# Optimization experiments

Hardware: AMD Instinct MI355X
Metric: run time of the kernel (lower is better)

## Reference

```python
import jax, jax.numpy as jnp
import numpy as np

B, S, ENC_H, DEC_H, ATTN = 64, 2048, 512, 512, 512


def setup_inputs() -> dict:
    key = jax.random.key(0)
    k1, k2, k3, k4, k5 = jax.random.split(key, 5)
    enc_outputs = jax.random.normal(k1, (B, S, ENC_H), dtype=jnp.float32)
    dec_hidden = jax.random.normal(k2, (B, DEC_H), dtype=jnp.float32)
    # nn.Linear(in, out, bias=False): weight shape [out, in]; y = x @ W.T
    s_enc = 1.0 / np.sqrt(ENC_H)
    s_dec = 1.0 / np.sqrt(DEC_H)
    s_v = 1.0 / np.sqrt(ATTN)
    W_enc = jax.random.uniform(k3, (ATTN, ENC_H), minval=-s_enc, maxval=s_enc, dtype=jnp.float32)
    W_dec = jax.random.uniform(k4, (ATTN, DEC_H), minval=-s_dec, maxval=s_dec, dtype=jnp.float32)
    v = jax.random.uniform(k5, (1, ATTN), minval=-s_v, maxval=s_v, dtype=jnp.float32)
    return {"enc_outputs": enc_outputs, "dec_hidden": dec_hidden,
            "W_enc": W_enc, "W_dec": W_dec, "v": v}


def reference(enc_outputs, dec_hidden, W_enc, W_dec, v):
    # enc_proj: [B,S,A], dec_proj: [B,1,A]
    enc_proj = jnp.einsum('bse,ae->bsa', enc_outputs, W_enc)
    dec_proj = jnp.einsum('bd,ad->ba', dec_hidden, W_dec)[:, None, :]
    score = jnp.einsum('bsa,a->bs', jnp.tanh(enc_proj + dec_proj), v[0])  # [B,S]
    attn_weights = jax.nn.softmax(score, axis=1)
    context = jnp.einsum('bs,bse->be', attn_weights, enc_outputs)  # [B,ENC_H]
    return (context, attn_weights)
```

## Files before the change

### kernel.cpp

```cpp
#include <hip/hip_runtime.h>
#include <hip/hip_bf16.h>

#define B_N 64
#define S_N 2048
#define E_N 512
#define A_N 512

typedef __bf16 bf16x8 __attribute__((ext_vector_type(8)));
typedef float  f32x4  __attribute__((ext_vector_type(4)));

__device__ __forceinline__ unsigned short f2bf(float f) {
  return __builtin_bit_cast(unsigned short, (__bf16)f);
}

__global__ void k_convw(const float* __restrict__ W, unsigned short* __restrict__ Wbf) {
  const int i = (blockIdx.x * 256 + threadIdx.x) * 4;
  const float4 v = *(const float4*)(W + i);
  ushort4 p;
  p.x = f2bf(v.x); p.y = f2bf(v.y); p.z = f2bf(v.z); p.w = f2bf(v.w);
  *(ushort4*)(Wbf + i) = p;
}

__global__ __launch_bounds__(256) void k_decproj(const float* __restrict__ dh,
                                                 const float* __restrict__ Wd,
                                                 float* __restrict__ decp) {
  const int b = blockIdx.x, tid = threadIdx.x;
  __shared__ float h[E_N];
  h[tid] = dh[b * E_N + tid];
  h[tid + 256] = dh[b * E_N + 256 + tid];
  __syncthreads();
  for (int a = tid; a < A_N; a += 256) {
    const float* wr = Wd + (size_t)a * E_N;
    float s = 0.f;
    #pragma unroll 8
    for (int e = 0; e < E_N; e += 4) {
      const float4 w4 = *(const float4*)(wr + e);
      s += w4.x * h[e] + w4.y * h[e + 1] + w4.z * h[e + 2] + w4.w * h[e + 3];
    }
    decp[b * A_N + a] = s;
  }
}

#define A_SZb   (64 * 128)
#define B_SZb   (512 * 128)
#define RED_OFF (A_SZb + B_SZb)
#define LDS_TOT (A_SZb + B_SZb + 4 * 64 * 4)

__device__ __forceinline__ int a_off(int r, int cb) {
  return r * 128 + (cb ^ ((r & 7) << 4));
}
__device__ __forceinline__ int b_off(int r, int cb) {
  return A_SZb + r * 128 + (cb ^ ((r & 7) << 4));
}

__global__ __launch_bounds__(256, 2) void k_scores(
    const float* __restrict__ enc, const unsigned short* __restrict__ Wbf,
    const float* __restrict__ decp, const float* __restrict__ vvec,
    float* __restrict__ scores) {
  __shared__ __align__(16) unsigned char lds[LDS_TOT];
  const int tid = threadIdx.x;
  const int lane = tid & 63, wv = tid >> 6, q = lane >> 4, ln = lane & 15;
  const int m0 = blockIdx.x * 64;
  const int b  = m0 >> 11;

  f32x4 acc[4][8] = {};

  for (int ks = 0; ks < 8; ++ks) {
    const int k0 = ks * 64;
    __syncthreads();
    {
      const float* Ag = enc + (size_t)m0 * E_N + k0;
      #pragma unroll
      for (int i = 0; i < 4; ++i) {
        const int idx = i * 256 + tid;
        const int row = idx >> 4, c = idx & 15;
        const float4 v4 = *(const float4*)(Ag + (size_t)row * E_N + c * 4);
        ushort4 p;
        p.x = f2bf(v4.x); p.y = f2bf(v4.y); p.z = f2bf(v4.z); p.w = f2bf(v4.w);
        *(ushort4*)(lds + a_off(row, c * 8)) = p;
      }
    }
    {
      const unsigned short* Wg = Wbf + k0;
      #pragma unroll
      for (int i = 0; i < 16; ++i) {
        const int idx = i * 256 + tid;
        const int row = idx >> 3, c = idx & 7;
        const uint4 v4 = *(const uint4*)(Wg + (size_t)row * A_N + c * 8);
        *(uint4*)(lds + b_off(row, c * 16)) = v4;
      }
    }
    __syncthreads();
    #pragma unroll
    for (int kt = 0; kt < 2; ++kt) {
      bf16x8 af[4], bfr[8];
      #pragma unroll
      for (int mt = 0; mt < 4; ++mt)
        af[mt] = *(const bf16x8*)(lds + a_off(mt * 16 + ln, kt * 64 + q * 16));
      #pragma unroll
      for (int nt = 0; nt < 8; ++nt)
        bfr[nt] = *(const bf16x8*)(lds + b_off(wv * 128 + nt * 16 + ln, kt * 64 + q * 16));
      #pragma unroll
      for (int mt = 0; mt < 4; ++mt) {
        #pragma unroll
        for (int nt = 0; nt < 8; ++nt)
          acc[mt][nt] = __builtin_amdgcn_mfma_f32_16x16x32_bf16(af[mt], bfr[nt], acc[mt][nt], 0, 0, 0);
      }
    }
  }

  float vv[8], dp[8];
  #pragma unroll
  for (int nt = 0; nt < 8; ++nt) {
    const int a = wv * 128 + nt * 16 + ln;
    vv[nt] = vvec[a];
    dp[nt] = decp[b * A_N + a];
  }
  float part[4][4] = {};
  #pragma unroll
  for (int mt = 0; mt < 4; ++mt) {
    #pragma unroll
    for (int nt = 0; nt < 8; ++nt) {
      #pragma unroll
      for (int r = 0; r < 4; ++r) {
        float x = acc[mt][nt][r] + dp[nt];
        x = fminf(9.f, fmaxf(-9.f, x));
        const float ex = __expf(2.f * x);
        part[mt][r] = fmaf(__fdividef(ex - 1.f, ex + 1.f), vv[nt], part[mt][r]);
      }
    }
  }
  float* red = (float*)(lds + RED_OFF);
  #pragma unroll
  for (int mt = 0; mt < 4; ++mt) {
    #pragma unroll
    for (int r = 0; r < 4; ++r) {
      float s = part[mt][r];
      s += __shfl_xor(s, 1);
      s += __shfl_xor(s, 2);
      s += __shfl_xor(s, 4);
      s += __shfl_xor(s, 8);
      if (ln == 0) red[wv * 64 + mt * 16 + q * 4 + r] = s;
    }
  }
  __syncthreads();
  if (tid < 64)
    scores[m0 + tid] = red[tid] + red[64 + tid] + red[128 + tid] + red[192 + tid];
}

__global__ __launch_bounds__(256) void k_softmax(const float* __restrict__ scores,
                                                 float* __restrict__ attn) {
  const int b = blockIdx.x, tid = threadIdx.x;
  float l[8];
  float mx = -3.4e38f;
  #pragma unroll
  for (int i = 0; i < 8; ++i) {
    l[i] = scores[b * S_N + i * 256 + tid];
    mx = fmaxf(mx, l[i]);
  }
  #pragma unroll
  for (int m = 1; m < 64; m <<= 1) mx = fmaxf(mx, __shfl_xor(mx, m));
  __shared__ float sred[8];
  if ((tid & 63) == 0) sred[tid >> 6] = mx;
  __syncthreads();
  mx = fmaxf(fmaxf(sred[0], sred[1]), fmaxf(sred[2], sred[3]));
  float se = 0.f;
  #pragma unroll
  for (int i = 0; i < 8; ++i) { l[i] = __expf(l[i] - mx); se += l[i]; }
  #pragma unroll
  for (int m = 1; m < 64; m <<= 1) se += __shfl_xor(se, m);
  if ((tid & 63) == 0) sred[4 + (tid >> 6)] = se;
  __syncthreads();
  se = sred[4] + sred[5] + sred[6] + sred[7];
  const float inv = 1.f / se;
  #pragma unroll
  for (int i = 0; i < 8; ++i) attn[b * S_N + i * 256 + tid] = l[i] * inv;
}

__global__ __launch_bounds__(512) void k_context(const float* __restrict__ enc,
                                                 const float* __restrict__ attn,
                                                 float* __restrict__ ctx) {
  const int blk = blockIdx.x;
  const int b = blk >> 2, eq = blk & 3;
  const int tid = threadIdx.x;
  const int te = tid & 31, sg = tid >> 5;
  const int e0 = eq * 128 + te * 4;
  const float* ep = enc + (size_t)b * S_N * E_N + e0;
  const float* wp = attn + b * S_N;
  f32x4 acc = {0.f, 0.f, 0.f, 0.f};
  const int s0 = sg * 128;
  #pragma unroll 4
  for (int s = s0; s < s0 + 128; ++s) {
    const float w = wp[s];
    const f32x4 ev = *(const f32x4*)(ep + (size_t)s * E_N);
    acc += w * ev;
  }
  __shared__ f32x4 red[16][32];
  red[sg][te] = acc;
  __syncthreads();
  if (sg == 0) {
    f32x4 t = red[0][te];
    #pragma unroll
    for (int g = 1; g < 16; ++g) t += red[g][te];
    *(f32x4*)(ctx + (size_t)b * E_N + e0) = t;
  }
}

extern "C" void kernel_launch(void* const* d_in, const int* in_sizes, int n_in,
                              void* d_out, int out_size, void* d_ws, size_t ws_size,
                              hipStream_t stream) {
  const float* enc = (const float*)d_in[0];
  const float* dh  = (const float*)d_in[1];
  const float* We  = (const float*)d_in[2];
  const float* Wd  = (const float*)d_in[3];
  const float* v   = (const float*)d_in[4];

  float* out_ctx  = (float*)d_out;
  float* out_attn = out_ctx + B_N * E_N;

  float* scores = (float*)d_ws;
  float* decp   = scores + B_N * S_N;
  unsigned short* Wbf = (unsigned short*)(decp + B_N * A_N);

  k_convw  <<<256, 256, 0, stream>>>(We, Wbf);
  k_decproj<<<B_N, 256, 0, stream>>>(dh, Wd, decp);
  k_scores <<<(B_N * S_N) / 64, 256, 0, stream>>>(enc, Wbf, decp, v, scores);
  k_softmax<<<B_N, 256, 0, stream>>>(scores, out_attn);
  k_context<<<B_N * 4, 512, 0, stream>>>(enc, out_attn, out_ctx);
}
```

Before: 211.7 us.

## Pre-pack W_enc into MFMA fragment layout and double-buffer the A tile

W_enc is now converted to bf16 directly in the per-lane MFMA operand order, so k_scores loads its B fragments straight from global memory (L2-resident) and no longer stages the 64KB weight tile through LDS each k-step. The encoder tile is double-buffered in LDS, with the next slice prefetched into registers while MFMAs run, which removes one barrier per iteration. Blocks grow to 512 threads (8 waves, each covering 64 attention columns), which shrinks the per-wave accumulators and LDS use. The cost is repeated global/L2 loads of the weight fragments by every block, plus more waves contending for them.

Result: slower. 227.2 us (+7.3%).

```diff
diff --git a/kernel.cpp b/kernel.cpp
--- a/kernel.cpp
+++ b/kernel.cpp
@@ -9,16 +9,25 @@
 typedef __bf16 bf16x8 __attribute__((ext_vector_type(8)));
 typedef float  f32x4  __attribute__((ext_vector_type(4)));
 
-__device__ __forceinline__ unsigned short f2bf(float f) {
-  return __builtin_bit_cast(unsigned short, (__bf16)f);
-}
-
-__global__ void k_convw(const float* __restrict__ W, unsigned short* __restrict__ Wbf) {
-  const int i = (blockIdx.x * 256 + threadIdx.x) * 4;
-  const float4 v = *(const float4*)(W + i);
-  ushort4 p;
-  p.x = f2bf(v.x); p.y = f2bf(v.y); p.z = f2bf(v.z); p.w = f2bf(v.w);
-  *(ushort4*)(Wbf + i) = p;
+__device__ __forceinline__ unsigned int f2bfu(float f) {
+  return (unsigned int)__builtin_bit_cast(unsigned short, (__bf16)f);
+}
+
+__global__ __launch_bounds__(256) void k_pack(const float* __restrict__ W,
+                                              unsigned short* __restrict__ Wp) {
+  const int pk = blockIdx.x * 256 + threadIdx.x;
+  const int l = pk & 63, k32 = (pk >> 6) & 15, c = pk >> 10;
+  const int ln = l & 15, q = l >> 4;
+  const int a = c * 16 + ln, k = k32 * 32 + q * 8;
+  const float* src = W + (size_t)a * E_N + k;
+  const float4 u = *(const float4*)src;
+  const float4 w = *(const float4*)(src + 4);
+  uint4 o;
+  o.x = f2bfu(u.x) | (f2bfu(u.y) << 16);
+  o.y = f2bfu(u.z) | (f2bfu(u.w) << 16);
+  o.z = f2bfu(w.x) | (f2bfu(w.y) << 16);
+  o.w = f2bfu(w.z) | (f2bfu(w.w) << 16);
+  *(uint4*)(Wp + (size_t)pk * 8) = o;
 }
 
 __global__ __launch_bounds__(256) void k_decproj(const float* __restrict__ dh,
@@ -41,20 +50,15 @@
   }
 }
 
-#define A_SZb   (64 * 128)
-#define B_SZb   (512 * 128)
-#define RED_OFF (A_SZb + B_SZb)
-#define LDS_TOT (A_SZb + B_SZb + 4 * 64 * 4)
-
-__device__ __forceinline__ int a_off(int r, int cb) {
-  return r * 128 + (cb ^ ((r & 7) << 4));
-}
-__device__ __forceinline__ int b_off(int r, int cb) {
-  return A_SZb + r * 128 + (cb ^ ((r & 7) << 4));
-}
-
-__global__ __launch_bounds__(256, 2) void k_scores(
-    const float* __restrict__ enc, const unsigned short* __restrict__ Wbf,
+#define RED_OFF (2 * 8192)
+#define LDS_TOT (2 * 8192 + 8 * 64 * 4)
+
+__device__ __forceinline__ int a_off(int p, int r, int cb) {
+  return p * 8192 + r * 128 + (cb ^ ((r & 7) << 4));
+}
+
+__global__ __launch_bounds__(512, 2) void k_scores(
+    const float* __restrict__ enc, const unsigned short* __restrict__ Wp,
     const float* __restrict__ decp, const float* __restrict__ vvec,
     float* __restrict__ scores) {
   __shared__ __align__(16) unsigned char lds[LDS_TOT];
@@ -62,65 +66,76 @@
   const int lane = tid & 63, wv = tid >> 6, q = lane >> 4, ln = lane & 15;
   const int m0 = blockIdx.x * 64;
   const int b  = m0 >> 11;
-
-  f32x4 acc[4][8] = {};
+  const bf16x8* __restrict__ Wp16 = (const bf16x8*)Wp;
+
+  const int srow = tid >> 3, sc8 = (tid & 7) * 8, scb = (tid & 7) * 16;
+  const float* Arow = enc + (size_t)m0 * E_N + (size_t)srow * E_N + sc8;
+
+  {
+    const float4 u = *(const float4*)Arow;
+    const float4 w = *(const float4*)(Arow + 4);
+    uint4 o;
+    o.x = f2bfu(u.x) | (f2bfu(u.y) << 16);
+    o.y = f2bfu(u.z) | (f2bfu(u.w) << 16);
+    o.z = f2bfu(w.x) | (f2bfu(w.y) << 16);
+    o.w = f2bfu(w.z) | (f2bfu(w.w) << 16);
+    *(uint4*)(lds + a_off(0, srow, scb)) = o;
+  }
+
+  f32x4 acc[4][4] = {};
 
   for (int ks = 0; ks < 8; ++ks) {
-    const int k0 = ks * 64;
     __syncthreads();
-    {
-      const float* Ag = enc + (size_t)m0 * E_N + k0;
-      #pragma unroll
-      for (int i = 0; i < 4; ++i) {
-        const int idx = i * 256 + tid;
-        const int row = idx >> 4, c = idx & 15;
-        const float4 v4 = *(const float4*)(Ag + (size_t)row * E_N + c * 4);
-        ushort4 p;
-        p.x = f2bf(v4.x); p.y = f2bf(v4.y); p.z = f2bf(v4.z); p.w = f2bf(v4.w);
-        *(ushort4*)(lds + a_off(row, c * 8)) = p;
+    const int p = ks & 1;
+    float4 u, w;
+    if (ks < 7) {
+      u = *(const float4*)(Arow + (ks + 1) * 64);
+      w = *(const float4*)(Arow + (ks + 1) * 64 + 4);
+    }
+    bf16x8 bfr[2][4];
+    #pragma unroll
+    for (int kt = 0; kt < 2; ++kt) {
+      #pragma unroll
+      for (int nt = 0; nt < 4; ++nt) {
+        const int c = wv * 4 + nt;
+        bfr[kt][nt] = Wp16[(c * 16 + ks * 2 + kt) * 64 + lane];
       }
     }
-    {
-      const unsigned short* Wg = Wbf + k0;
-      #pragma unroll
-      for (int i = 0; i < 16; ++i) {
-        const int idx = i * 256 + tid;
-        const int row = idx >> 3, c = idx & 7;
-        const uint4 v4 = *(const uint4*)(Wg + (size_t)row * A_N + c * 8);
-        *(uint4*)(lds + b_off(row, c * 16)) = v4;
-      }
-    }
-    __syncthreads();
-    #pragma unroll
-    for (int kt = 0; kt < 2; ++kt) {
-      bf16x8 af[4], bfr[8];
+    bf16x8 afr[2][4];
+    #pragma unroll
+    for (int kt = 0; kt < 2; ++kt)
       #pragma unroll
       for (int mt = 0; mt < 4; ++mt)
-        af[mt] = *(const bf16x8*)(lds + a_off(mt * 16 + ln, kt * 64 + q * 16));
-      #pragma unroll
-      for (int nt = 0; nt < 8; ++nt)
-        bfr[nt] = *(const bf16x8*)(lds + b_off(wv * 128 + nt * 16 + ln, kt * 64 + q * 16));
-      #pragma unroll
-      for (int mt = 0; mt < 4; ++mt) {
+        afr[kt][mt] = *(const bf16x8*)(lds + a_off(p, mt * 16 + ln, kt * 64 + q * 16));
+    #pragma unroll
+    for (int kt = 0; kt < 2; ++kt)
+      #pragma unroll
+      for (int mt = 0; mt < 4; ++mt)
         #pragma unroll
-        for (int nt = 0; nt < 8; ++nt)
-          acc[mt][nt] = __builtin_amdgcn_mfma_f32_16x16x32_bf16(af[mt], bfr[nt], acc[mt][nt], 0, 0, 0);
-      }
-    }
-  }
-
-  float vv[8], dp[8];
-  #pragma unroll
-  for (int nt = 0; nt < 8; ++nt) {
-    const int a = wv * 128 + nt * 16 + ln;
+        for (int nt = 0; nt < 4; ++nt)
+          acc[mt][nt] = __builtin_amdgcn_mfma_f32_16x16x32_bf16(afr[kt][mt], bfr[kt][nt], acc[mt][nt], 0, 0, 0);
+    if (ks < 7) {
+      uint4 o;
+      o.x = f2bfu(u.x) | (f2bfu(u.y) << 16);
+      o.y = f2bfu(u.z) | (f2bfu(u.w) << 16);
+      o.z = f2bfu(w.x) | (f2bfu(w.y) << 16);
+      o.w = f2bfu(w.z) | (f2bfu(w.w) << 16);
+      *(uint4*)(lds + a_off(p ^ 1, srow, scb)) = o;
+    }
+  }
+
+  float vv[4], dp[4];
+  #pragma unroll
+  for (int nt = 0; nt < 4; ++nt) {
+    const int a = wv * 64 + nt * 16 + ln;
     vv[nt] = vvec[a];
     dp[nt] = decp[b * A_N + a];
   }
   float part[4][4] = {};
   #pragma unroll
-  for (int mt = 0; mt < 4; ++mt) {
-    #pragma unroll
-    for (int nt = 0; nt < 8; ++nt) {
+  for (int mt = 0; mt < 4; ++mt)
+    #pragma unroll
+    for (int nt = 0; nt < 4; ++nt)
       #pragma unroll
       for (int r = 0; r < 4; ++r) {
         float x = acc[mt][nt][r] + dp[nt];
@@ -128,11 +143,9 @@
         const float ex = __expf(2.f * x);
         part[mt][r] = fmaf(__fdividef(ex - 1.f, ex + 1.f), vv[nt], part[mt][r]);
       }
-    }
-  }
   float* red = (float*)(lds + RED_OFF);
   #pragma unroll
-  for (int mt = 0; mt < 4; ++mt) {
+  for (int mt = 0; mt < 4; ++mt)
     #pragma unroll
     for (int r = 0; r < 4; ++r) {
       float s = part[mt][r];
@@ -142,10 +155,13 @@
       s += __shfl_xor(s, 8);
       if (ln == 0) red[wv * 64 + mt * 16 + q * 4 + r] = s;
     }
-  }
-  __syncthreads();
-  if (tid < 64)
-    scores[m0 + tid] = red[tid] + red[64 + tid] + red[128 + tid] + red[192 + tid];
+  __syncthreads();
+  if (tid < 64) {
+    float s = 0.f;
+    #pragma unroll
+    for (int w8 = 0; w8 < 8; ++w8) s += red[w8 * 64 + tid];
+    scores[m0 + tid] = s;
+  }
 }
 
 __global__ __launch_bounds__(256) void k_softmax(const float* __restrict__ scores,
@@ -220,11 +236,11 @@
 
   float* scores = (float*)d_ws;
   float* decp   = scores + B_N * S_N;
-  unsigned short* Wbf = (unsigned short*)(decp + B_N * A_N);
-
-  k_convw  <<<256, 256, 0, stream>>>(We, Wbf);
+  unsigned short* Wp = (unsigned short*)(decp + B_N * A_N);
+
+  k_pack   <<<128, 256, 0, stream>>>(We, Wp);
   k_decproj<<<B_N, 256, 0, stream>>>(dh, Wd, decp);
-  k_scores <<<(B_N * S_N) / 64, 256, 0, stream>>>(enc, Wbf, decp, v, scores);
+  k_scores <<<(B_N * S_N) / 64, 512, 0, stream>>>(enc, Wp, decp, v, scores);
   k_softmax<<<B_N, 256, 0, stream>>>(scores, out_attn);
   k_context<<<B_N * 4, 512, 0, stream>>>(enc, out_attn, out_ctx);
 }
```
